# Kernel tuning notes

Measured on AMD Instinct MI355X. Metric: run time of the kernel, lower is better.

The kernel has to match this reference:

```python
import jax, jax.numpy as jnp
import numpy as np

N = 20000      # nodes (spots)
D = 256        # embed_dim
H = 4          # n_heads
DH = D // H    # head dim
L = 2          # n_layers
E = 320000     # edges (avg degree 16)
K = 48         # static padded-neighbor cap (>= true max degree for this data)
EPS = 1e-5
NEG = -1e30


def setup_inputs() -> dict:
    key = jax.random.key(0)
    ks = jax.random.split(key, 8)
    s = 0.05
    return {
        "expr_embed": jax.random.normal(ks[0], (N, D), jnp.float32),
        "spatial_embed": jax.random.normal(ks[1], (N, D), jnp.float32),
        "in_proj_w": jax.random.normal(ks[2], (L, 3 * D, D), jnp.float32) * s,
        "in_proj_b": jnp.zeros((L, 3 * D), jnp.float32),
        "out_proj_w": jax.random.normal(ks[3], (L, D, D), jnp.float32) * s,
        "out_proj_b": jnp.zeros((L, D), jnp.float32),
        "ffn_w1": jax.random.normal(ks[4], (L, 2 * D, D), jnp.float32) * s,
        "ffn_b1": jnp.zeros((L, 2 * D), jnp.float32),
        "ffn_w2": jax.random.normal(ks[5], (L, D, 2 * D), jnp.float32) * s,
        "ffn_b2": jnp.zeros((L, D), jnp.float32),
        "ln1_g": jnp.ones((L, D), jnp.float32),
        "ln1_b": jnp.zeros((L, D), jnp.float32),
        "ln2_g": jnp.ones((L, D), jnp.float32),
        "ln2_b": jnp.zeros((L, D), jnp.float32),
        "edge_index": jax.random.randint(ks[6], (2, E), 0, N, jnp.int32),
    }


def _build_neighbors(edge_index):
    """Padded neighbor indices (N,K) and key_padding_mask (N,K) (True = pad)."""
    src, tgt = edge_index[0], edge_index[1]
    counts = jnp.zeros((N,), jnp.int32).at[tgt].add(1)
    order = jnp.argsort(tgt)                       # group edges by target
    src_s, tgt_s = src[order], tgt[order]
    offsets = jnp.concatenate([jnp.zeros((1,), jnp.int32),
                               jnp.cumsum(counts)[:-1].astype(jnp.int32)])
    pos = jnp.arange(E, dtype=jnp.int32) - offsets[tgt_s]
    pos = jnp.where(pos < K, pos, K)               # K is out-of-bounds -> dropped
    nbr = jnp.zeros((N, K), jnp.int32).at[tgt_s, pos].set(src_s, mode='drop')
    pad = jnp.ones((N, K), bool).at[tgt_s, pos].set(False, mode='drop')
    iso = counts == 0                              # isolated spots attend to self
    nbr = nbr.at[:, 0].set(jnp.where(iso, jnp.arange(N, dtype=jnp.int32), nbr[:, 0]))
    pad = pad.at[:, 0].set(jnp.where(iso, False, pad[:, 0]))
    return nbr, pad


def _layernorm(x, g, b):
    mu = jnp.mean(x, -1, keepdims=True)
    var = jnp.var(x, -1, keepdims=True)
    return (x - mu) * jax.lax.rsqrt(var + EPS) * g + b


def _forward(expr_embed, spatial_embed, in_proj_w, in_proj_b, out_proj_w,
             out_proj_b, ffn_w1, ffn_b1, ffn_w2, ffn_b2,
             ln1_g, ln1_b, ln2_g, ln2_b, nbr, pad):
    x = expr_embed
    scale = 1.0 / jnp.sqrt(jnp.asarray(DH, x.dtype))
    for i in range(L):
        Wq, Wk, Wv = jnp.split(in_proj_w[i], 3, axis=0)
        bq, bk, bv = jnp.split(in_proj_b[i], 3, axis=0)
        q = (x @ Wq.T + bq).reshape(N, H, DH)
        # project spatial once, gather projected rows (same math as gather-then-project)
        k = (spatial_embed @ Wk.T + bk)[nbr].reshape(N, K, H, DH)
        v = (spatial_embed @ Wv.T + bv)[nbr].reshape(N, K, H, DH)
        scores = jnp.einsum('nhd,nkhd->nhk', q, k) * scale      # (N,H,K)
        scores = jnp.where(pad[:, None, :], NEG, scores)
        attn = jax.nn.softmax(scores, axis=-1)
        ao = jnp.einsum('nhk,nkhd->nhd', attn, v).reshape(N, D)
        ao = ao @ out_proj_w[i].T + out_proj_b[i]
        x = _layernorm(x + ao, ln1_g[i], ln1_b[i])
        h = jax.nn.gelu(x @ ffn_w1[i].T + ffn_b1[i], approximate=False)
        h = h @ ffn_w2[i].T + ffn_b2[i]
        x = _layernorm(x + h, ln2_g[i], ln2_b[i])
    return x


def reference(expr_embed, spatial_embed, in_proj_w, in_proj_b, out_proj_w,
              out_proj_b, ffn_w1, ffn_b1, ffn_w2, ffn_b2,
              ln1_g, ln1_b, ln2_g, ln2_b, edge_index):
    nbr, pad = _build_neighbors(edge_index.astype(jnp.int32))
    return _forward(expr_embed, spatial_embed, in_proj_w, in_proj_b, out_proj_w,
                    out_proj_b, ffn_w1, ffn_b1, ffn_w2, ffn_b2,
                    ln1_g, ln1_b, ln2_g, ln2_b, nbr, pad)
```

## Files before the change

### kernel.cpp

```cpp
#include <hip/hip_runtime.h>

#define N_NODES 20000
#define DIM 256
#define NHEAD 4
#define DHEAD 64
#define NLAYER 2
#define NEDGE 320000
#define KCAP 48
#define NBM64 313

typedef __bf16 v8bf __attribute__((ext_vector_type(8)));
typedef float v4f __attribute__((ext_vector_type(4)));

union LU { uint4 u; v8bf v; };

__device__ __forceinline__ unsigned short f2bf(float f) {
    unsigned u = __float_as_uint(f);
    unsigned r = u + 0x7FFFu + ((u >> 16) & 1u);
    return (unsigned short)(r >> 16);
}
__device__ __forceinline__ float bflo(unsigned u) { return __uint_as_float(u << 16); }
__device__ __forceinline__ float bfhi(unsigned u) { return __uint_as_float(u & 0xFFFF0000u); }

__global__ void sniff_kernel(const unsigned short* __restrict__ p,
                             int* __restrict__ flag) {
    __shared__ int s;
    if (threadIdx.x == 0) s = 0;
    __syncthreads();
    int c = 0;
    for (int i = threadIdx.x; i < 4096; i += 256) {
        unsigned short u = p[i];
        unsigned e = (u >> 7) & 0xFFu;
        if (e == 0xFFu) c++;
        else if (e == 0u && (u & 0x7Fu)) c++;
    }
    atomicAdd(&s, c);
    __syncthreads();
    if (threadIdx.x == 0) flag[0] = (s >= 4) ? 1 : 0;
}

struct ConvBfArgs { const void* src[4]; unsigned short* dst[4]; int n[4]; };

__global__ void conv_bf16_kernel(ConvBfArgs a, const int* __restrict__ flag) {
    const int t  = blockIdx.y;
    const int n  = a.n[t];
    const int i0 = (blockIdx.x * 256 + threadIdx.x) * 4;
    if (i0 >= n) return;
    unsigned short* dst = a.dst[t];
    if (flag[0]) {
        float4 v = *(const float4*)((const float*)a.src[t] + i0);
        ushort4 o;
        o.x = f2bf(v.x); o.y = f2bf(v.y); o.z = f2bf(v.z); o.w = f2bf(v.w);
        *(ushort4*)(dst + i0) = o;
    } else {
        ushort4 u = *(const ushort4*)((const unsigned short*)a.src[t] + i0);
        *(ushort4*)(dst + i0) = u;
    }
}

struct ConvF32Args { const void* src[8]; float* dst[8]; int n[8]; };

__global__ void conv_f32_kernel(ConvF32Args a, const int* __restrict__ flag) {
    const int t  = blockIdx.y;
    const int n  = a.n[t];
    const int i0 = (blockIdx.x * 256 + threadIdx.x) * 4;
    if (i0 >= n) return;
    float* dst = a.dst[t];
    if (flag[0]) {
        float4 v = *(const float4*)((const float*)a.src[t] + i0);
        *(float4*)(dst + i0) = v;
    } else {
        ushort4 u = *(const ushort4*)((const unsigned short*)a.src[t] + i0);
        *(float4*)(dst + i0) = make_float4(bflo(u.x), bflo(u.y), bflo(u.z), bflo(u.w));
    }
}

__global__ void zero_cnt_kernel(int* __restrict__ cnt) {
    int i = blockIdx.x * 256 + threadIdx.x;
    if (i < N_NODES) cnt[i] = 0;
}

__global__ void build_nbr_kernel(const int* __restrict__ ei,
                                 int* __restrict__ cnt, int* __restrict__ nbr) {
    int e = blockIdx.x * 256 + threadIdx.x;
    if (e >= NEDGE) return;
    int s = ei[e];
    int t = ei[NEDGE + e];
    int slot = atomicAdd(&cnt[t], 1);
    if (slot < KCAP) nbr[t * KCAP + slot] = s;
}

__global__ __launch_bounds__(256) void gemm_kernel(
    const unsigned short* __restrict__ A, const unsigned short* __restrict__ B,
    const float* __restrict__ bias, unsigned short* __restrict__ C,
    int M, int Nc, int Kd, int do_gelu)
{
    __shared__ __align__(16) __bf16 As[64][72];
    __shared__ __align__(16) __bf16 Bs[128][72];
    const int tid  = threadIdx.x;
    const int m0   = blockIdx.x * 64;
    const int n0   = blockIdx.y * 128;
    const int wave = tid >> 6;
    const int lane = tid & 63;
    const int wn0  = wave * 32;
    const int lm   = lane & 15;
    const int lk   = (lane >> 4) * 8;

    v4f acc[4][2] = {};

    for (int k0 = 0; k0 < Kd; k0 += 64) {
#pragma unroll
        for (int i = 0; i < 2; ++i) {
            int c   = tid + i * 256;
            int row = c >> 3;
            int col = (c & 7) << 3;
            uint4 u = make_uint4(0u, 0u, 0u, 0u);
            if (m0 + row < M)
                u = *(const uint4*)&A[(size_t)(m0 + row) * Kd + k0 + col];
            LU ta; ta.u = u;
            *(v8bf*)&As[row][col] = ta.v;
        }
#pragma unroll
        for (int i = 0; i < 4; ++i) {
            int c   = tid + i * 256;
            int row = c >> 3;
            int col = (c & 7) << 3;
            LU tb; tb.u = *(const uint4*)&B[(size_t)(n0 + row) * Kd + k0 + col];
            *(v8bf*)&Bs[row][col] = tb.v;
        }
        __syncthreads();
#pragma unroll
        for (int ks = 0; ks < 2; ++ks) {
            v8bf af[4], bq[2];
#pragma unroll
            for (int mi = 0; mi < 4; ++mi)
                af[mi] = *(const v8bf*)&As[mi * 16 + lm][ks * 32 + lk];
#pragma unroll
            for (int ni = 0; ni < 2; ++ni)
                bq[ni] = *(const v8bf*)&Bs[wn0 + ni * 16 + lm][ks * 32 + lk];
#pragma unroll
            for (int mi = 0; mi < 4; ++mi)
#pragma unroll
                for (int ni = 0; ni < 2; ++ni)
                    acc[mi][ni] = __builtin_amdgcn_mfma_f32_16x16x32_bf16(
                        af[mi], bq[ni], acc[mi][ni], 0, 0, 0);
        }
        __syncthreads();
    }

    const int rq = (lane >> 4) << 2;
#pragma unroll
    for (int ni = 0; ni < 2; ++ni) {
        int col  = n0 + wn0 + ni * 16 + lm;
        float bv = bias[col];
#pragma unroll
        for (int mi = 0; mi < 4; ++mi) {
#pragma unroll
            for (int r = 0; r < 4; ++r) {
                int row = m0 + mi * 16 + rq + r;
                if (row >= M) continue;
                float v = acc[mi][ni][r] + bv;
                if (do_gelu) v = 0.5f * v * (1.0f + erff(v * 0.7071067811865475f));
                C[(size_t)row * Nc + col] = f2bf(v);
            }
        }
    }
}

__global__ __launch_bounds__(256) void attn_kernel(
    const unsigned short* __restrict__ q,
    const unsigned short* __restrict__ kv,
    const int* __restrict__ nbr,
    const int* __restrict__ cnt,
    unsigned short* __restrict__ ao)
{
    const int n    = blockIdx.x;
    const int tid  = threadIdx.x;
    const int h    = tid >> 6;
    const int lane = tid & 63;

    __shared__ float sc[NHEAD][KCAP];
    __shared__ int   nbs[KCAP];

    int deg = cnt[n];
    if (deg > KCAP) deg = KCAP;
    const bool iso = (deg == 0);
    if (iso) deg = 1;

    if (tid < KCAP)
        nbs[tid] = (tid < deg) ? (iso ? n : nbr[n * KCAP + tid]) : 0;
    __syncthreads();

    {
        const int sub = lane & 7;
        const int grp = lane >> 3;
        float qf[8];
        {
            uint4 qu = *(const uint4*)&q[(size_t)n * DIM + h * DHEAD + sub * 8];
            qf[0] = bflo(qu.x); qf[1] = bfhi(qu.x);
            qf[2] = bflo(qu.y); qf[3] = bfhi(qu.y);
            qf[4] = bflo(qu.z); qf[5] = bfhi(qu.z);
            qf[6] = bflo(qu.w); qf[7] = bfhi(qu.w);
        }
        const int nit = (deg + 7) >> 3;
        for (int it = 0; it < nit; ++it) {
            int j  = it * 8 + grp;
            int jc = (j < deg) ? j : (deg - 1);
            int nb = nbs[jc];
            uint4 ku = *(const uint4*)&kv[(size_t)nb * 512 + h * DHEAD + sub * 8];
            float p = qf[0] * bflo(ku.x);
            p = fmaf(qf[1], bfhi(ku.x), p);
            p = fmaf(qf[2], bflo(ku.y), p);
            p = fmaf(qf[3], bfhi(ku.y), p);
            p = fmaf(qf[4], bflo(ku.z), p);
            p = fmaf(qf[5], bfhi(ku.z), p);
            p = fmaf(qf[6], bflo(ku.w), p);
            p = fmaf(qf[7], bfhi(ku.w), p);
            p += __shfl_xor(p, 1, 64);
            p += __shfl_xor(p, 2, 64);
            p += __shfl_xor(p, 4, 64);
            if (sub == 0 && j < deg) sc[h][j] = p * 0.125f;
        }
    }
    __syncthreads();

    {
        float s  = (lane < deg) ? sc[h][lane] : -1e30f;
        float mx = s;
#pragma unroll
        for (int m = 32; m >= 1; m >>= 1) mx = fmaxf(mx, __shfl_xor(mx, m, 64));
        float e   = (lane < deg) ? __expf(s - mx) : 0.0f;
        float sum = e;
#pragma unroll
        for (int m = 32; m >= 1; m >>= 1) sum += __shfl_xor(sum, m, 64);
        float inv = 1.0f / sum;
        if (lane < KCAP) sc[h][lane] = e * inv;
    }
    __syncthreads();

    {
        const int quarter = lane >> 4;
        const int d0      = (lane & 15) * 4;
        float a0 = 0.f, a1 = 0.f, a2 = 0.f, a3 = 0.f;
        for (int j = 0; j < deg; j += 4) {
            int j0 = j + quarter;
            int jc = (j0 < deg) ? j0 : (deg - 1);
            int nb = nbs[jc];
            uint2 u = *(const uint2*)&kv[(size_t)nb * 512 + 256 + h * DHEAD + d0];
            float w = (j0 < deg) ? sc[h][j0] : 0.f;
            a0 = fmaf(w, bflo(u.x), a0);
            a1 = fmaf(w, bfhi(u.x), a1);
            a2 = fmaf(w, bflo(u.y), a2);
            a3 = fmaf(w, bfhi(u.y), a3);
        }
        a0 += __shfl_xor(a0, 16, 64); a0 += __shfl_xor(a0, 32, 64);
        a1 += __shfl_xor(a1, 16, 64); a1 += __shfl_xor(a1, 32, 64);
        a2 += __shfl_xor(a2, 16, 64); a2 += __shfl_xor(a2, 32, 64);
        a3 += __shfl_xor(a3, 16, 64); a3 += __shfl_xor(a3, 32, 64);
        if (lane < 16) {
            uint2 o;
            o.x = (unsigned)f2bf(a0) | ((unsigned)f2bf(a1) << 16);
            o.y = (unsigned)f2bf(a2) | ((unsigned)f2bf(a3) << 16);
            *(uint2*)&ao[(size_t)n * DIM + h * DHEAD + d0] = o;
        }
    }
}

__global__ __launch_bounds__(256) void ln_add_kernel(
    const unsigned short* __restrict__ x, const unsigned short* __restrict__ t,
    const float* __restrict__ g, const float* __restrict__ b,
    unsigned short* __restrict__ xout, void* __restrict__ dout,
    int final_out, const int* __restrict__ flag)
{
    const int wave = threadIdx.x >> 6;
    const int lane = threadIdx.x & 63;
    const int row  = blockIdx.x * 4 + wave;

    const ushort4 xu = *(const ushort4*)&x[(size_t)row * DIM + lane * 4];
    const ushort4 tu = *(const ushort4*)&t[(size_t)row * DIM + lane * 4];
    float v[4];
    v[0] = bflo(xu.x) + bflo(tu.x);
    v[1] = bflo(xu.y) + bflo(tu.y);
    v[2] = bflo(xu.z) + bflo(tu.z);
    v[3] = bflo(xu.w) + bflo(tu.w);

    float s = 0.f, ss = 0.f;
#pragma unroll
    for (int i = 0; i < 4; ++i) { s += v[i]; ss += v[i] * v[i]; }
#pragma unroll
    for (int m = 32; m >= 1; m >>= 1) {
        s  += __shfl_xor(s, m, 64);
        ss += __shfl_xor(ss, m, 64);
    }
    const float mu  = s * (1.0f / DIM);
    const float var = ss * (1.0f / DIM) - mu * mu;
    const float r   = rsqrtf(var + 1e-5f);

    float o[4];
#pragma unroll
    for (int i = 0; i < 4; ++i) {
        int c = lane * 4 + i;
        o[i] = (v[i] - mu) * r * g[c] + b[c];
    }
    if (final_out) {
        if (flag[0]) {
            *(float4*)&((float*)dout)[(size_t)row * DIM + lane * 4] =
                make_float4(o[0], o[1], o[2], o[3]);
        } else {
            ushort4 u;
            u.x = f2bf(o[0]); u.y = f2bf(o[1]); u.z = f2bf(o[2]); u.w = f2bf(o[3]);
            *(ushort4*)&((unsigned short*)dout)[(size_t)row * DIM + lane * 4] = u;
        }
    } else {
        ushort4 u;
        u.x = f2bf(o[0]); u.y = f2bf(o[1]); u.z = f2bf(o[2]); u.w = f2bf(o[3]);
        *(ushort4*)&xout[(size_t)row * DIM + lane * 4] = u;
    }
}

extern "C" void kernel_launch(void* const* d_in, const int* in_sizes, int n_in,
                              void* d_out, int out_size, void* d_ws, size_t ws_size,
                              hipStream_t stream) {
    const int* ei = (const int*)d_in[14];

    char* ws = (char*)d_ws;
    size_t off = 0;
    auto alloc = [&](size_t bytes) -> void* {
        void* p = ws + off;
        off = (off + bytes + 255) & ~(size_t)255;
        return p;
    };

    ConvBfArgs ce;
    unsigned short* expr_b = (unsigned short*)alloc((size_t)N_NODES * DIM * 2);
    unsigned short* spat_b = (unsigned short*)alloc((size_t)N_NODES * DIM * 2);
    ce.src[0] = d_in[0]; ce.dst[0] = expr_b; ce.n[0] = N_NODES * DIM;
    ce.src[1] = d_in[1]; ce.dst[1] = spat_b; ce.n[1] = N_NODES * DIM;
    ce.src[2] = d_in[0]; ce.dst[2] = expr_b; ce.n[2] = 0;
    ce.src[3] = d_in[0]; ce.dst[3] = expr_b; ce.n[3] = 0;

    const int widx[4] = { 2, 4, 6, 8 };
    const int wn[4]   = { NLAYER * 3 * DIM * DIM, NLAYER * DIM * DIM,
                          NLAYER * 2 * DIM * DIM, NLAYER * DIM * 2 * DIM };
    ConvBfArgs cw;
    unsigned short* canw[4];
    for (int i = 0; i < 4; ++i) {
        canw[i] = (unsigned short*)alloc((size_t)wn[i] * 2);
        cw.src[i] = d_in[widx[i]];
        cw.dst[i] = canw[i];
        cw.n[i]   = wn[i];
    }
    const unsigned short* ipw = canw[0];
    const unsigned short* opw = canw[1];
    const unsigned short* w1  = canw[2];
    const unsigned short* w2  = canw[3];

    const int fidx[8] = { 3, 5, 7, 9, 10, 11, 12, 13 };
    const int fn[8]   = { NLAYER * 3 * DIM, NLAYER * DIM, NLAYER * 2 * DIM,
                          NLAYER * DIM, NLAYER * DIM, NLAYER * DIM,
                          NLAYER * DIM, NLAYER * DIM };
    ConvF32Args cf;
    float* canf[8];
    for (int i = 0; i < 8; ++i) {
        canf[i] = (float*)alloc((size_t)fn[i] * 4);
        cf.src[i] = d_in[fidx[i]];
        cf.dst[i] = canf[i];
        cf.n[i]   = fn[i];
    }

    unsigned short* x_buf  = (unsigned short*)alloc((size_t)N_NODES * DIM * 2);
    unsigned short* q_buf  = (unsigned short*)alloc((size_t)N_NODES * DIM * 2);
    unsigned short* kv_buf = (unsigned short*)alloc((size_t)N_NODES * 2 * DIM * 2);
    unsigned short* ao_buf = (unsigned short*)alloc((size_t)N_NODES * DIM * 2);
    unsigned short* h_buf  = (unsigned short*)alloc((size_t)N_NODES * 2 * DIM * 2);
    unsigned short* t_buf  = (unsigned short*)alloc((size_t)N_NODES * DIM * 2);
    int* cnt  = (int*)alloc((size_t)N_NODES * 4);
    int* nbr  = (int*)alloc((size_t)N_NODES * KCAP * 4);
    int* flag = (int*)alloc(256);

    sniff_kernel<<<1, 256, 0, stream>>>((const unsigned short*)d_in[0], flag);
    conv_bf16_kernel<<<dim3((N_NODES * DIM) / 1024, 2), 256, 0, stream>>>(ce, flag);
    conv_bf16_kernel<<<dim3((wn[0] + 1023) / 1024, 4), 256, 0, stream>>>(cw, flag);
    conv_f32_kernel<<<dim3(2, 8), 256, 0, stream>>>(cf, flag);
    zero_cnt_kernel<<<(N_NODES + 255) / 256, 256, 0, stream>>>(cnt);
    build_nbr_kernel<<<(NEDGE + 255) / 256, 256, 0, stream>>>(ei, cnt, nbr);

    for (int i = 0; i < NLAYER; ++i) {
        const unsigned short* Wqkv = ipw + (size_t)i * 3 * DIM * DIM;
        const float*          bqkv = canf[0] + (size_t)i * 3 * DIM;
        const unsigned short* xin  = (i == 0) ? expr_b : x_buf;

        gemm_kernel<<<dim3(NBM64, 2), 256, 0, stream>>>(
            xin, Wqkv, bqkv, q_buf, N_NODES, DIM, DIM, 0);
        gemm_kernel<<<dim3(NBM64, 4), 256, 0, stream>>>(
            spat_b, Wqkv + (size_t)DIM * DIM, bqkv + DIM, kv_buf,
            N_NODES, 2 * DIM, DIM, 0);
        attn_kernel<<<N_NODES, 256, 0, stream>>>(q_buf, kv_buf, nbr, cnt, ao_buf);
        gemm_kernel<<<dim3(NBM64, 2), 256, 0, stream>>>(
            ao_buf, opw + (size_t)i * DIM * DIM, canf[1] + (size_t)i * DIM,
            t_buf, N_NODES, DIM, DIM, 0);
        ln_add_kernel<<<N_NODES / 4, 256, 0, stream>>>(
            xin, t_buf, canf[4] + (size_t)i * DIM, canf[5] + (size_t)i * DIM,
            x_buf, nullptr, 0, flag);
        gemm_kernel<<<dim3(NBM64, 4), 256, 0, stream>>>(
            x_buf, w1 + (size_t)i * 2 * DIM * DIM, canf[2] + (size_t)i * 2 * DIM,
            h_buf, N_NODES, 2 * DIM, DIM, 1);
        gemm_kernel<<<dim3(NBM64, 2), 256, 0, stream>>>(
            h_buf, w2 + (size_t)i * DIM * 2 * DIM, canf[3] + (size_t)i * DIM,
            t_buf, N_NODES, DIM, 2 * DIM, 0);
        ln_add_kernel<<<N_NODES / 4, 256, 0, stream>>>(
            x_buf, t_buf, canf[6] + (size_t)i * DIM, canf[7] + (size_t)i * DIM,
            x_buf, d_out, (i == NLAYER - 1) ? 1 : 0, flag);
    }
}
```

Measured before the change: 482.6 us.

## Prefetch GEMM tiles into registers, fuse Q and KV projections, merge conversions

The GEMM body now loads the next K-tile from global memory into registers while the current tile is used for MFMA, so load latency overlaps compute. The separate Q and KV projection GEMMs are merged into one launch whose grid y index selects the input, weight slice and output buffer. The two bf16 conversion launches are combined into a single 6-way launch. This cuts launch count and exposed load latency at the cost of more registers per thread.

```diff
diff --git a/kernel.cpp b/kernel.cpp
--- a/kernel.cpp
+++ b/kernel.cpp
@@ -39,7 +39,7 @@
     if (threadIdx.x == 0) flag[0] = (s >= 4) ? 1 : 0;
 }
 
-struct ConvBfArgs { const void* src[4]; unsigned short* dst[4]; int n[4]; };
+struct ConvBfArgs { const void* src[6]; unsigned short* dst[6]; int n[6]; };
 
 __global__ void conv_bf16_kernel(ConvBfArgs a, const int* __restrict__ flag) {
     const int t  = blockIdx.y;
@@ -90,6 +90,99 @@
     if (slot < KCAP) nbr[t * KCAP + slot] = s;
 }
 
+__device__ __forceinline__ void gemm_body(
+    __bf16 (*As)[72], __bf16 (*Bs)[72],
+    const unsigned short* __restrict__ A, const unsigned short* __restrict__ B,
+    const float* __restrict__ bias, unsigned short* __restrict__ C,
+    int M, int Nc, int Kd, int m0, int nB, int nC, int do_gelu)
+{
+    const int tid  = threadIdx.x;
+    const int wave = tid >> 6;
+    const int lane = tid & 63;
+    const int wn0  = wave * 32;
+    const int lm   = lane & 15;
+    const int lk   = (lane >> 4) * 8;
+    const int srow = tid >> 3;
+    const int scol = (tid & 7) << 3;
+
+    uint4 pa[2], pb[4];
+#pragma unroll
+    for (int i = 0; i < 2; ++i) {
+        int row = srow + i * 32;
+        pa[i] = make_uint4(0u, 0u, 0u, 0u);
+        if (m0 + row < M)
+            pa[i] = *(const uint4*)&A[(size_t)(m0 + row) * Kd + scol];
+    }
+#pragma unroll
+    for (int i = 0; i < 4; ++i) {
+        int row = srow + i * 32;
+        pb[i] = *(const uint4*)&B[(size_t)(nB + row) * Kd + scol];
+    }
+
+    v4f acc[4][2] = {};
+
+    for (int k0 = 0; k0 < Kd; k0 += 64) {
+#pragma unroll
+        for (int i = 0; i < 2; ++i) { LU t; t.u = pa[i]; *(v8bf*)&As[srow + i * 32][scol] = t.v; }
+#pragma unroll
+        for (int i = 0; i < 4; ++i) { LU t; t.u = pb[i]; *(v8bf*)&Bs[srow + i * 32][scol] = t.v; }
+        __syncthreads();
+
+        const int kn = k0 + 64;
+        if (kn < Kd) {
+#pragma unroll
+            for (int i = 0; i < 2; ++i) {
+                int row = srow + i * 32;
+                pa[i] = make_uint4(0u, 0u, 0u, 0u);
+                if (m0 + row < M)
+                    pa[i] = *(const uint4*)&A[(size_t)(m0 + row) * Kd + kn + scol];
+            }
+#pragma unroll
+            for (int i = 0; i < 4; ++i) {
+                int row = srow + i * 32;
+                pb[i] = *(const uint4*)&B[(size_t)(nB + row) * Kd + kn + scol];
+            }
+        }
+
+#pragma unroll
+        for (int ks = 0; ks < 2; ++ks) {
+            v8bf af[4], bq[2];
+#pragma unroll
+            for (int mi = 0; mi < 4; ++mi)
+                af[mi] = *(const v8bf*)&As[mi * 16 + lm][ks * 32 + lk];
+#pragma unroll
+            for (int ni = 0; ni < 2; ++ni)
+                bq[ni] = *(const v8bf*)&Bs[wn0 + ni * 16 + lm][ks * 32 + lk];
+#pragma unroll
+            for (int mi = 0; mi < 4; ++mi)
+#pragma unroll
+                for (int ni = 0; ni < 2; ++ni)
+                    acc[mi][ni] = __builtin_amdgcn_mfma_f32_16x16x32_bf16(
+                        af[mi], bq[ni], acc[mi][ni], 0, 0, 0);
+        }
+        __syncthreads();
+    }
+
+    const int rq = (lane >> 4) << 2;
+#pragma unroll
+    for (int ni = 0; ni < 2; ++ni) {
+        int colb = wn0 + ni * 16 + lm;
+        float bv = bias[nB + colb];
+        int colc = nC + colb;
+#pragma unroll
+        for (int mi = 0; mi < 4; ++mi) {
+#pragma unroll
+            for (int r = 0; r < 4; ++r) {
+                int row = m0 + mi * 16 + rq + r;
+                if (row >= M) continue;
+                float v = acc[mi][ni][r] + bv;
+                if (do_gelu) v = 0.5f * v * (1.0f + erff(v * 0.7071067811865475f));
+                C[(size_t)row * Nc + colc] = f2bf(v);
+            }
+        }
+    }
+}
+
 __global__ __launch_bounds__(256) void gemm_kernel(
     const unsigned short* __restrict__ A, const unsigned short* __restrict__ B,
     const float* __restrict__ bias, unsigned short* __restrict__ C,
@@ -97,74 +190,24 @@
 {
     __shared__ __align__(16) __bf16 As[64][72];
     __shared__ __align__(16) __bf16 Bs[128][72];
-    const int tid  = threadIdx.x;
-    const int m0   = blockIdx.x * 64;
-    const int n0   = blockIdx.y * 128;
-    const int wave = tid >> 6;
-    const int lane = tid & 63;
-    const int wn0  = wave * 32;
-    const int lm   = lane & 15;
-    const int lk   = (lane >> 4) * 8;
-
-    v4f acc[4][2] = {};
-
-    for (int k0 = 0; k0 < Kd; k0 += 64) {
-#pragma unroll
-        for (int i = 0; i < 2; ++i) {
-            int c   = tid + i * 256;
-            int row = c >> 3;
-            int col = (c & 7) << 3;
-            uint4 u = make_uint4(0u, 0u, 0u, 0u);
-            if (m0 + row < M)
-                u = *(const uint4*)&A[(size_t)(m0 + row) * Kd + k0 + col];
-            LU ta; ta.u = u;
-            *(v8bf*)&As[row][col] = ta.v;
-        }
-#pragma unroll
-        for (int i = 0; i < 4; ++i) {
-            int c   = tid + i * 256;
-            int row = c >> 3;
-            int col = (c & 7) << 3;
-            LU tb; tb.u = *(const uint4*)&B[(size_t)(n0 + row) * Kd + k0 + col];
-            *(v8bf*)&Bs[row][col] = tb.v;
-        }
-        __syncthreads();
-#pragma unroll
-        for (int ks = 0; ks < 2; ++ks) {
-            v8bf af[4], bq[2];
-#pragma unroll
-            for (int mi = 0; mi < 4; ++mi)
-                af[mi] = *(const v8bf*)&As[mi * 16 + lm][ks * 32 + lk];
-#pragma unroll
-            for (int ni = 0; ni < 2; ++ni)
-                bq[ni] = *(const v8bf*)&Bs[wn0 + ni * 16 + lm][ks * 32 + lk];
-#pragma unroll
-            for (int mi = 0; mi < 4; ++mi)
-#pragma unroll
-                for (int ni = 0; ni < 2; ++ni)
-                    acc[mi][ni] = __builtin_amdgcn_mfma_f32_16x16x32_bf16(
-                        af[mi], bq[ni], acc[mi][ni], 0, 0, 0);
-        }
-        __syncthreads();
-    }
-
-    const int rq = (lane >> 4) << 2;
-#pragma unroll
-    for (int ni = 0; ni < 2; ++ni) {
-        int col  = n0 + wn0 + ni * 16 + lm;
-        float bv = bias[col];
-#pragma unroll
-        for (int mi = 0; mi < 4; ++mi) {
-#pragma unroll
-            for (int r = 0; r < 4; ++r) {
-                int row = m0 + mi * 16 + rq + r;
-                if (row >= M) continue;
-                float v = acc[mi][ni][r] + bv;
-                if (do_gelu) v = 0.5f * v * (1.0f + erff(v * 0.7071067811865475f));
-                C[(size_t)row * Nc + col] = f2bf(v);
-            }
-        }
-    }
+    const int n0 = blockIdx.y * 128;
+    gemm_body(As, Bs, A, B, bias, C, M, Nc, Kd, blockIdx.x * 64, n0, n0, do_gelu);
+}
+
+__global__ __launch_bounds__(256) void qkv_kernel(
+    const unsigned short* __restrict__ x, const unsigned short* __restrict__ spat,
+    const unsigned short* __restrict__ W, const float* __restrict__ bias,
+    unsigned short* __restrict__ q, unsigned short* __restrict__ kv, int M)
+{
+    __shared__ __align__(16) __bf16 As[64][72];
+    __shared__ __align__(16) __bf16 Bs[128][72];
+    const int y = blockIdx.y;
+    const unsigned short* A = (y < 2) ? x : spat;
+    unsigned short*       C = (y < 2) ? q : kv;
+    const int Nc = (y < 2) ? 256 : 512;
+    const int nB = y * 128;
+    const int nC = (y < 2) ? nB : nB - 256;
+    gemm_body(As, Bs, A, W, bias, C, M, Nc, 256, blockIdx.x * 64, nB, nC, 0);
 }
 
 __global__ __launch_bounds__(256) void attn_kernel(
@@ -331,29 +374,24 @@
         return p;
     };
 
-    ConvBfArgs ce;
-    unsigned short* expr_b = (unsigned short*)alloc((size_t)N_NODES * DIM * 2);
-    unsigned short* spat_b = (unsigned short*)alloc((size_t)N_NODES * DIM * 2);
-    ce.src[0] = d_in[0]; ce.dst[0] = expr_b; ce.n[0] = N_NODES * DIM;
-    ce.src[1] = d_in[1]; ce.dst[1] = spat_b; ce.n[1] = N_NODES * DIM;
-    ce.src[2] = d_in[0]; ce.dst[2] = expr_b; ce.n[2] = 0;
-    ce.src[3] = d_in[0]; ce.dst[3] = expr_b; ce.n[3] = 0;
-
-    const int widx[4] = { 2, 4, 6, 8 };
-    const int wn[4]   = { NLAYER * 3 * DIM * DIM, NLAYER * DIM * DIM,
+    const int bidx[6] = { 0, 1, 2, 4, 6, 8 };
+    const int bnn[6]  = { N_NODES * DIM, N_NODES * DIM,
+                          NLAYER * 3 * DIM * DIM, NLAYER * DIM * DIM,
                           NLAYER * 2 * DIM * DIM, NLAYER * DIM * 2 * DIM };
-    ConvBfArgs cw;
-    unsigned short* canw[4];
-    for (int i = 0; i < 4; ++i) {
-        canw[i] = (unsigned short*)alloc((size_t)wn[i] * 2);
-        cw.src[i] = d_in[widx[i]];
-        cw.dst[i] = canw[i];
-        cw.n[i]   = wn[i];
-    }
-    const unsigned short* ipw = canw[0];
-    const unsigned short* opw = canw[1];
-    const unsigned short* w1  = canw[2];
-    const unsigned short* w2  = canw[3];
+    ConvBfArgs cb;
+    unsigned short* canb[6];
+    for (int i = 0; i < 6; ++i) {
+        canb[i] = (unsigned short*)alloc((size_t)bnn[i] * 2);
+        cb.src[i] = d_in[bidx[i]];
+        cb.dst[i] = canb[i];
+        cb.n[i]   = bnn[i];
+    }
+    const unsigned short* expr_b = canb[0];
+    const unsigned short* spat_b = canb[1];
+    const unsigned short* ipw    = canb[2];
+    const unsigned short* opw    = canb[3];
+    const unsigned short* w1     = canb[4];
+    const unsigned short* w2     = canb[5];
 
     const int fidx[8] = { 3, 5, 7, 9, 10, 11, 12, 13 };
     const int fn[8]   = { NLAYER * 3 * DIM, NLAYER * DIM, NLAYER * 2 * DIM,
@@ -379,8 +417,7 @@
     int* flag = (int*)alloc(256);
 
     sniff_kernel<<<1, 256, 0, stream>>>((const unsigned short*)d_in[0], flag);
-    conv_bf16_kernel<<<dim3((N_NODES * DIM) / 1024, 2), 256, 0, stream>>>(ce, flag);
-    conv_bf16_kernel<<<dim3((wn[0] + 1023) / 1024, 4), 256, 0, stream>>>(cw, flag);
+    conv_bf16_kernel<<<dim3((N_NODES * DIM) / 1024, 6), 256, 0, stream>>>(cb, flag);
     conv_f32_kernel<<<dim3(2, 8), 256, 0, stream>>>(cf, flag);
     zero_cnt_kernel<<<(N_NODES + 255) / 256, 256, 0, stream>>>(cnt);
     build_nbr_kernel<<<(NEDGE + 255) / 256, 256, 0, stream>>>(ei, cnt, nbr);
@@ -390,11 +427,8 @@
         const float*          bqkv = canf[0] + (size_t)i * 3 * DIM;
         const unsigned short* xin  = (i == 0) ? expr_b : x_buf;
 
-        gemm_kernel<<<dim3(NBM64, 2), 256, 0, stream>>>(
-            xin, Wqkv, bqkv, q_buf, N_NODES, DIM, DIM, 0);
-        gemm_kernel<<<dim3(NBM64, 4), 256, 0, stream>>>(
-            spat_b, Wqkv + (size_t)DIM * DIM, bqkv + DIM, kv_buf,
-            N_NODES, 2 * DIM, DIM, 0);
+        qkv_kernel<<<dim3(NBM64, 6), 256, 0, stream>>>(
+            xin, spat_b, Wqkv, bqkv, q_buf, kv_buf, N_NODES);
         attn_kernel<<<N_NODES, 256, 0, stream>>>(q_buf, kv_buf, nbr, cnt, ao_buf);
         gemm_kernel<<<dim3(NBM64, 2), 256, 0, stream>>>(
             ao_buf, opw + (size_t)i * DIM * DIM, canf[1] + (size_t)i * DIM,
```

Measured after the change: 449.4 us. -6.9%, faster.
